# Optimization experiments

Hardware: AMD Instinct MI355X
Metric: run time of the kernel (lower is better)

Reference implementation:

```python
import jax, jax.numpy as jnp
import numpy as np

N, L, C, H, W, HEAD = 16, 256, 512, 32, 32, 16

def setup_inputs() -> dict:
    key = jax.random.key(0)
    ks = jax.random.split(key, 8)
    s = 0.02  # weight init scale
    return {
        "feature": jax.random.normal(ks[0], (N, C, H, W), jnp.float32),
        "token": jax.random.normal(ks[1], (N, L, C), jnp.float32),
        "wq": jax.random.normal(ks[2], (C, C), jnp.float32) * s,
        "bq": jax.random.normal(ks[3], (C,), jnp.float32) * s,
        "wk": jax.random.normal(ks[4], (C, C), jnp.float32) * s,
        "bk": jax.random.normal(ks[5], (C,), jnp.float32) * s,
        "wv": jax.random.normal(ks[6], (C, C), jnp.float32) * s,
        "bv": jax.random.normal(ks[7], (C,), jnp.float32) * s,
    }

def reference(feature, token, wq, bq, wk, bk, wv, bv):
    n, c, hgt, wid = feature.shape
    h = HEAD
    d = c // h
    l = token.shape[1]
    scale = jnp.asarray(np.sqrt(c / h), feature.dtype)
    tok = token.transpose(0, 2, 1)  # (N, C, L)
    # 1x1 conv projections == per-position GEMMs
    v = (jnp.einsum('ncl,dc->ndl', tok, wv) + bv[None, :, None]).reshape(n, h, d, l)
    k = (jnp.einsum('ncl,dc->ndl', tok, wk) + bk[None, :, None]).reshape(n, h, d, l)
    q = (jnp.einsum('nchw,dc->ndhw', feature, wq) + bq[None, :, None, None])
    q = q.reshape(n, h, d, hgt * wid).transpose(0, 1, 3, 2)  # (N, h, HW, d)
    scores = jnp.einsum('nhqd,nhdl->nhql', q, k) / scale  # (N, h, HW, L)
    coef = jax.nn.softmax(scores, axis=-1)
    proj = jnp.einsum('nhdl,nhql->nhdq', v, coef)  # (N, h, d, HW)
    return feature + proj.reshape(n, c, hgt, wid)
```

## Files before the change

kernel.cpp:

```cpp
#include <hip/hip_runtime.h>
#include <hip/hip_bf16.h>

#define N_ 16
#define L_ 256
#define C_ 512
#define HW_ 1024
#define HEADS_ 16
#define DH_ 32

typedef unsigned short u16;
typedef unsigned int u32;
typedef __attribute__((ext_vector_type(8))) short short8_t;
typedef __attribute__((ext_vector_type(4))) float f32x4;

__device__ __forceinline__ u16 f2bs(float f) {
    union { float f; u32 i; } x; x.f = f;
    u32 r = x.i + 0x7fffu + ((x.i >> 16) & 1u);
    return (u16)(r >> 16);
}
__device__ __forceinline__ u32 cvt_pk_bf16(float lo, float hi) {
    u32 r;
    asm("v_cvt_pk_bf16_f32 %0, %1, %2" : "=v"(r) : "v"(lo), "v"(hi));
    return r;
}
#define AS1(p) (const __attribute__((address_space(1))) void*)(p)
#define AS3(p) (__attribute__((address_space(3))) void*)(p)

__global__ __launch_bounds__(256) void prep_kernel(
    const float* __restrict__ token, const float* __restrict__ wq,
    const float* __restrict__ wk, const float* __restrict__ wv,
    const float* __restrict__ feature,
    u16* __restrict__ tokb, u16* __restrict__ wqb,
    u16* __restrict__ wkb, u16* __restrict__ wvb,
    u16* __restrict__ Ftb)
{
    __shared__ float LT[64][67];
    const int t = threadIdx.x;

    if (blockIdx.x < 2816) {
        const int idx = blockIdx.x * 256 + t;
        const float* s; u16* d; int off;
        if (idx < 524288)            { s = token; d = tokb; off = idx; }
        else if (idx < 524288+65536) { s = wq; d = wqb; off = idx - 524288; }
        else if (idx < 524288+131072){ s = wk; d = wkb; off = idx - 524288 - 65536; }
        else                         { s = wv; d = wvb; off = idx - 524288 - 131072; }
        float4 v = ((const float4*)s)[off];
        ushort4 w;
        w.x = f2bs(v.x); w.y = f2bs(v.y); w.z = f2bs(v.z); w.w = f2bs(v.w);
        ((ushort4*)d)[off] = w;
    } else {
        const int tidx = blockIdx.x - 2816;
        const int pb = tidx & 15, cb = (tidx >> 4) & 7, n = tidx >> 7;
        const int c0 = cb * 64, pos0 = pb * 64;

        #pragma unroll
        for (int r = 0; r < 4; ++r) {
            const int c = r * 16 + (t >> 4);
            const int p = (t & 15) * 4;
            float4 v = *(const float4*)&feature[
                ((size_t)n * C_ + c0 + c) * HW_ + pos0 + p];
            LT[c][p] = v.x; LT[c][p+1] = v.y; LT[c][p+2] = v.z; LT[c][p+3] = v.w;
        }
        __syncthreads();
        #pragma unroll
        for (int rep = 0; rep < 2; ++rep) {
            const int pos = (t >> 3) + rep * 32;
            const int c = (t & 7) * 8;
            u16 tmp[8];
            #pragma unroll
            for (int j = 0; j < 8; ++j) tmp[j] = f2bs(LT[c + j][pos]);
            *(short8_t*)&Ftb[(size_t)(n * HW_ + pos0 + pos) * C_ + c0 + c] =
                *(short8_t*)tmp;
        }
    }
}

__global__ __launch_bounds__(256) void gemm_kernel(
    const u16* __restrict__ Ftb, const u16* __restrict__ tokb,
    const u16* __restrict__ wqb, const u16* __restrict__ wkb,
    const u16* __restrict__ wvb,
    const float* __restrict__ bq, const float* __restrict__ bk,
    const float* __restrict__ bv,
    u16* __restrict__ Qout, u16* __restrict__ Kout, u16* __restrict__ Vt)
{
    __shared__ __align__(16) unsigned char smem[32768];

    const int t = threadIdx.x;
    const int lane = t & 63, wid = t >> 6;
    const int i16 = lane & 15, g = lane >> 4;
    const int wm = wid >> 1, wn = wid & 1;
    const int r8 = t >> 3, gr = t & 7;

    if (blockIdx.x < 256) {
        const int xcd = blockIdx.x & 7, j = blockIdx.x >> 3;
        const int m0 = (xcd * 4 + (j & 3)) * 128;
        const int n0 = (j >> 2) * 64;
        u16* Tok = (u16*)smem;
        u16* Bk  = (u16*)(smem + 16384);
        u16* Bv  = (u16*)(smem + 24576);
        u16 (*LTo)[72] = (u16(*)[72])smem;

        f32x4 ak[4][2], av[4][2];
        #pragma unroll
        for (int mt = 0; mt < 4; ++mt)
            #pragma unroll
            for (int nt = 0; nt < 2; ++nt) {
                ak[mt][nt] = (f32x4){0.f, 0.f, 0.f, 0.f};
                av[mt][nt] = (f32x4){0.f, 0.f, 0.f, 0.f};
            }

        for (int c0 = 0; c0 < C_; c0 += 64) {
            __syncthreads();
            #pragma unroll
            for (int p = 0; p < 4; ++p) {
                const int row = p * 32 + r8;
                __builtin_amdgcn_global_load_lds(
                    AS1(tokb + (size_t)(m0 + row) * C_ + c0 + ((gr ^ (row & 7)) << 3)),
                    AS3(smem + (p * 32 + wid * 8) * 128), 16, 0, 0);
            }
            #pragma unroll
            for (int p = 0; p < 2; ++p) {
                const int row = p * 32 + r8;
                const int gs = (gr ^ (row & 7)) << 3;
                __builtin_amdgcn_global_load_lds(
                    AS1(wkb + (size_t)(n0 + row) * C_ + c0 + gs),
                    AS3(smem + 16384 + (p * 32 + wid * 8) * 128), 16, 0, 0);
                __builtin_amdgcn_global_load_lds(
                    AS1(wvb + (size_t)(n0 + row) * C_ + c0 + gs),
                    AS3(smem + 24576 + (p * 32 + wid * 8) * 128), 16, 0, 0);
            }
            __syncthreads();
            #pragma unroll
            for (int ks = 0; ks < 2; ++ks) {
                short8_t a[4], bbk[2], bbv[2];
                #pragma unroll
                for (int mt = 0; mt < 4; ++mt) {
                    const int m = wm * 64 + mt * 16 + i16;
                    a[mt] = *(const short8_t*)&Tok[m * 64 + ((((ks << 2) | g) ^ (m & 7)) << 3)];
                }
                #pragma unroll
                for (int nt = 0; nt < 2; ++nt) {
                    const int d = wn * 32 + nt * 16 + i16;
                    const int sw = d * 64 + ((((ks << 2) | g) ^ (d & 7)) << 3);
                    bbk[nt] = *(const short8_t*)&Bk[sw];
                    bbv[nt] = *(const short8_t*)&Bv[sw];
                }
                #pragma unroll
                for (int mt = 0; mt < 4; ++mt)
                    #pragma unroll
                    for (int nt = 0; nt < 2; ++nt) {
                        ak[mt][nt] = __builtin_amdgcn_mfma_f32_16x16x32_bf16(
                            a[mt], bbk[nt], ak[mt][nt], 0, 0, 0);
                        av[mt][nt] = __builtin_amdgcn_mfma_f32_16x16x32_bf16(
                            a[mt], bbv[nt], av[mt][nt], 0, 0, 0);
                    }
            }
        }
        const int nb = m0 >> 8, l0 = m0 & 255;
        const size_t vtbase = (size_t)nb * C_ * L_;
        #pragma unroll
        for (int nt = 0; nt < 2; ++nt) {
            const int d = n0 + wn * 32 + nt * 16 + i16;
            const float bb = bv[d];
            #pragma unroll
            for (int mt = 0; mt < 4; ++mt) {
                ushort4 w;
                w.x = f2bs(av[mt][nt][0] + bb);
                w.y = f2bs(av[mt][nt][1] + bb);
                w.z = f2bs(av[mt][nt][2] + bb);
                w.w = f2bs(av[mt][nt][3] + bb);
                const int l = l0 + wm * 64 + mt * 16 + g * 4;
                *(ushort4*)&Vt[vtbase + (size_t)d * L_ + l] = w;
            }
        }
        __syncthreads();
        #pragma unroll
        for (int nt = 0; nt < 2; ++nt) {
            const int col = wn * 32 + nt * 16 + i16;
            const float bb = bk[n0 + col];
            #pragma unroll
            for (int mt = 0; mt < 4; ++mt)
                #pragma unroll
                for (int r = 0; r < 4; ++r)
                    LTo[wm * 64 + mt * 16 + g * 4 + r][col] = f2bs(ak[mt][nt][r] + bb);
        }
        __syncthreads();
        #pragma unroll
        for (int rep = 0; rep < 4; ++rep) {
            const int m = (t >> 3) + rep * 32;
            const int cs = (t & 7) * 8;
            *(short8_t*)&Kout[(size_t)(m0 + m) * C_ + n0 + cs] = *(short8_t*)&LTo[m][cs];
        }
    } else {
        const int qid = blockIdx.x - 256;
        const int xcd = qid & 7, j = qid >> 3;
        const int m0 = (xcd * 16 + (j & 15)) * 128;
        const int n0 = (j >> 4) * 64;
        u16* Ft = (u16*)smem;
        u16* Bq = (u16*)(smem + 16384);
        u16 (*LTo)[72] = (u16(*)[72])smem;

        f32x4 aq[4][2];
        #pragma unroll
        for (int mt = 0; mt < 4; ++mt)
            #pragma unroll
            for (int nt = 0; nt < 2; ++nt)
                aq[mt][nt] = (f32x4){0.f, 0.f, 0.f, 0.f};

        for (int c0 = 0; c0 < C_; c0 += 64) {
            __syncthreads();
            #pragma unroll
            for (int p = 0; p < 4; ++p) {
                const int row = p * 32 + r8;
                __builtin_amdgcn_global_load_lds(
                    AS1(Ftb + (size_t)(m0 + row) * C_ + c0 + ((gr ^ (row & 7)) << 3)),
                    AS3(smem + (p * 32 + wid * 8) * 128), 16, 0, 0);
            }
            #pragma unroll
            for (int p = 0; p < 2; ++p) {
                const int row = p * 32 + r8;
                __builtin_amdgcn_global_load_lds(
                    AS1(wqb + (size_t)(n0 + row) * C_ + c0 + ((gr ^ (row & 7)) << 3)),
                    AS3(smem + 16384 + (p * 32 + wid * 8) * 128), 16, 0, 0);
            }
            __syncthreads();
            #pragma unroll
            for (int ks = 0; ks < 2; ++ks) {
                short8_t a[4], b[2];
                #pragma unroll
                for (int mt = 0; mt < 4; ++mt) {
                    const int m = wm * 64 + mt * 16 + i16;
                    a[mt] = *(const short8_t*)&Ft[m * 64 + ((((ks << 2) | g) ^ (m & 7)) << 3)];
                }
                #pragma unroll
                for (int nt = 0; nt < 2; ++nt) {
                    const int d = wn * 32 + nt * 16 + i16;
                    b[nt] = *(const short8_t*)&Bq[d * 64 + ((((ks << 2) | g) ^ (d & 7)) << 3)];
                }
                #pragma unroll
                for (int mt = 0; mt < 4; ++mt)
                    #pragma unroll
                    for (int nt = 0; nt < 2; ++nt)
                        aq[mt][nt] = __builtin_amdgcn_mfma_f32_16x16x32_bf16(
                            a[mt], b[nt], aq[mt][nt], 0, 0, 0);
            }
        }
        __syncthreads();
        #pragma unroll
        for (int nt = 0; nt < 2; ++nt) {
            const int col = wn * 32 + nt * 16 + i16;
            const float bb = bq[n0 + col];
            #pragma unroll
            for (int mt = 0; mt < 4; ++mt)
                #pragma unroll
                for (int r = 0; r < 4; ++r)
                    LTo[wm * 64 + mt * 16 + g * 4 + r][col] = f2bs(aq[mt][nt][r] + bb);
        }
        __syncthreads();
        #pragma unroll
        for (int rep = 0; rep < 4; ++rep) {
            const int m = (t >> 3) + rep * 32;
            const int cs = (t & 7) * 8;
            *(short8_t*)&Qout[(size_t)(m0 + m) * C_ + n0 + cs] = *(short8_t*)&LTo[m][cs];
        }
    }
}

__global__ __launch_bounds__(256) void attn_kernel(
    const u16* __restrict__ Qws, const u16* __restrict__ Kws,
    const u16* __restrict__ Vws, const float* __restrict__ feature,
    float* __restrict__ out)
{
    __shared__ __align__(16) unsigned char smem[32768];

    const int t = threadIdx.x;
    const int wid = t >> 6, lane = t & 63;
    const int i16 = lane & 15, g = lane >> 4;
    const int pt = blockIdx.x, h = blockIdx.y, n = blockIdx.z;
    const int pos0 = pt * 64;
    const size_t qbase = ((size_t)n * HW_ + pos0) * C_ + h * DH_;
    const size_t kbase = ((size_t)n * L_) * C_ + h * DH_;
    const size_t vbase = (size_t)n * C_ * L_ + (size_t)h * DH_ * L_;

    const int q = wid * 16 + i16;

    short8_t bq = *(const short8_t*)&Qws[qbase + (size_t)q * C_ + g * 8];

    #pragma unroll
    for (int p = 0; p < 4; ++p) {
        const int kg = (lane & 3) ^ ((lane >> 3) & 3);
        const int kr = wid * 64 + p * 16 + (lane >> 2);
        const u16* ksrc = Kws + kbase + (size_t)kr * C_ + kg * 8;
        __builtin_amdgcn_global_load_lds(AS1(ksrc),
            AS3(smem + wid * 4096 + p * 1024), 16, 0, 0);
        const int vd = wid * 8 + p * 2 + (lane >> 5);
        const u16* vsrc = Vws + vbase + (size_t)vd * L_ + ((lane & 31) ^ (vd & 7)) * 8;
        __builtin_amdgcn_global_load_lds(AS1(vsrc),
            AS3(smem + 16384 + wid * 4096 + p * 1024), 16, 0, 0);
    }
    __syncthreads();

    const int kgr = g ^ ((i16 >> 1) & 3);
    f32x4 s[16];
    #pragma unroll
    for (int nf = 0; nf < 16; ++nf) {
        short8_t a = *(const short8_t*)(smem + (nf * 16 + i16) * 64 + kgr * 16);
        f32x4 z = {0.f, 0.f, 0.f, 0.f};
        s[nf] = __builtin_amdgcn_mfma_f32_16x16x32_bf16(a, bq, z, 0, 0, 0);
    }

    float mm[16], sm[16];
    #pragma unroll
    for (int nf = 0; nf < 16; ++nf)
        mm[nf] = fmaxf(fmaxf(s[nf][0], s[nf][1]), fmaxf(s[nf][2], s[nf][3]));
    #pragma unroll
    for (int st = 8; st >= 1; st >>= 1)
        #pragma unroll
        for (int i = 0; i < 8; ++i)
            if (i < st) mm[i] = fmaxf(mm[i], mm[i + st]);
    float m = mm[0];
    m = fmaxf(m, __shfl_xor(m, 16));
    m = fmaxf(m, __shfl_xor(m, 32));

    const float K2 = 0.25506288f;
    #pragma unroll
    for (int nf = 0; nf < 16; ++nf) {
        #pragma unroll
        for (int r = 0; r < 4; ++r) s[nf][r] = exp2f((s[nf][r] - m) * K2);
        sm[nf] = (s[nf][0] + s[nf][1]) + (s[nf][2] + s[nf][3]);
    }
    #pragma unroll
    for (int st = 8; st >= 1; st >>= 1)
        #pragma unroll
        for (int i = 0; i < 8; ++i)
            if (i < st) sm[i] += sm[i + st];
    float ssum = sm[0];
    ssum += __shfl_xor(ssum, 16);
    ssum += __shfl_xor(ssum, 32);
    const float pinv = 1.0f / ssum;

    __syncthreads();

    f32x4 o0 = {0.f, 0.f, 0.f, 0.f}, o1 = {0.f, 0.f, 0.f, 0.f};
    const int e7 = i16 & 7;

    #pragma unroll
    for (int hb = 0; hb < 2; ++hb) {
        #pragma unroll
        for (int nfp = 0; nfp < 8; ++nfp) {
            const int nf = hb * 8 + nfp;
            #pragma unroll
            for (int w = 0; w < 2; ++w) {
                u32 pw = cvt_pk_bf16(s[nf][2 * w] * pinv, s[nf][2 * w + 1] * pinv);
                const int gran = (nfp * 2 + (g >> 1)) ^ e7;
                *(u32*)(smem + q * 256 + gran * 16 + ((g & 1) * 2 + w) * 4) = pw;
            }
        }
        __syncthreads();
        #pragma unroll
        for (int ks = 0; ks < 4; ++ks) {
            short8_t pb = *(const short8_t*)(smem + q * 256 + (((ks * 4 + g) ^ e7) * 16));
            const int vg = (((hb * 4 + ks) * 4 + g) ^ e7) * 16;
            short8_t va0 = *(const short8_t*)(smem + 16384 + i16 * 512 + vg);
            short8_t va1 = *(const short8_t*)(smem + 16384 + (16 + i16) * 512 + vg);
            o0 = __builtin_amdgcn_mfma_f32_16x16x32_bf16(va0, pb, o0, 0, 0, 0);
            o1 = __builtin_amdgcn_mfma_f32_16x16x32_bf16(va1, pb, o1, 0, 0, 0);
        }
        if (hb == 0) __syncthreads();
    }

    const size_t obase = ((size_t)n * C_ + h * DH_) * HW_ + pos0 + q;
    #pragma unroll
    for (int r = 0; r < 4; ++r) {
        const size_t oa = obase + (size_t)(g * 4 + r) * HW_;
        out[oa] = feature[oa] + o0[r];
        const size_t ob = obase + (size_t)(16 + g * 4 + r) * HW_;
        out[ob] = feature[ob] + o1[r];
    }
}

extern "C" void kernel_launch(void* const* d_in, const int* in_sizes, int n_in,
                              void* d_out, int out_size, void* d_ws, size_t ws_size,
                              hipStream_t stream)
{
    const float* feature = (const float*)d_in[0];
    const float* token   = (const float*)d_in[1];
    const float* wq      = (const float*)d_in[2];
    const float* bq      = (const float*)d_in[3];
    const float* wk      = (const float*)d_in[4];
    const float* bk      = (const float*)d_in[5];
    const float* wv      = (const float*)d_in[6];
    const float* bv      = (const float*)d_in[7];
    float* out = (float*)d_out;

    u16* Qws = (u16*)d_ws;
    u16* Kws = Qws + (size_t)N_ * HW_ * C_;
    u16* Vws = Kws + (size_t)N_ * L_ * C_;

    char* ob = (char*)d_out;
    u16* Ftb  = (u16*)ob;
    u16* tokb = (u16*)(ob + (16u << 20));
    u16* wkb  = (u16*)(ob + (20u << 20));
    u16* wvb  = (u16*)(ob + (20u << 20) + 524288);
    u16* wqb  = (u16*)(ob + (21u << 20));

    prep_kernel<<<dim3(4864), 256, 0, stream>>>(token, wq, wk, wv, feature,
                                                tokb, wqb, wkb, wvb, Ftb);
    gemm_kernel<<<dim3(1280), 256, 0, stream>>>(Ftb, tokb, wqb, wkb, wvb,
                                                bq, bk, bv, Qws, Kws, Vws);
    attn_kernel<<<dim3(16, 16, 16), 256, 0, stream>>>(Qws, Kws, Vws, feature, out);
}
```

Baseline: 71.04 us.

## Double-buffer LDS staging in projection GEMM and widen Q tiles to 128

The K/V and Q projection loops now use two 32KB LDS buffers. The next 64-wide channel slice is issued with global_load_lds while MFMAs run on the current slice, which removes one barrier per iteration and hides load latency. The Q branch also doubles its output tile width from 64 to 128 columns, with 16 accumulators per wave. This halves the number of Q blocks (1024 to 512, grid 1280 to 768) and improves reuse of the feature tile. In exchange, LDS per block doubles to 64KB and register pressure rises, which lowers occupancy, and the Q epilogue is split into two halves through LDS.

```diff
diff --git a/kernel.cpp b/kernel.cpp
--- a/kernel.cpp
+++ b/kernel.cpp
@@ -83,21 +83,18 @@
     const float* __restrict__ bv,
     u16* __restrict__ Qout, u16* __restrict__ Kout, u16* __restrict__ Vt)
 {
-    __shared__ __align__(16) unsigned char smem[32768];
+    __shared__ __align__(16) unsigned char smem[65536];
 
     const int t = threadIdx.x;
     const int lane = t & 63, wid = t >> 6;
     const int i16 = lane & 15, g = lane >> 4;
-    const int wm = wid >> 1, wn = wid & 1;
     const int r8 = t >> 3, gr = t & 7;
 
     if (blockIdx.x < 256) {
         const int xcd = blockIdx.x & 7, j = blockIdx.x >> 3;
         const int m0 = (xcd * 4 + (j & 3)) * 128;
         const int n0 = (j >> 2) * 64;
-        u16* Tok = (u16*)smem;
-        u16* Bk  = (u16*)(smem + 16384);
-        u16* Bv  = (u16*)(smem + 24576);
+        const int wm = wid >> 1, wn = wid & 1;
         u16 (*LTo)[72] = (u16(*)[72])smem;
 
         f32x4 ak[4][2], av[4][2];
@@ -109,27 +106,33 @@
                 av[mt][nt] = (f32x4){0.f, 0.f, 0.f, 0.f};
             }
 
-        for (int c0 = 0; c0 < C_; c0 += 64) {
-            __syncthreads();
-            #pragma unroll
-            for (int p = 0; p < 4; ++p) {
-                const int row = p * 32 + r8;
-                __builtin_amdgcn_global_load_lds(
-                    AS1(tokb + (size_t)(m0 + row) * C_ + c0 + ((gr ^ (row & 7)) << 3)),
-                    AS3(smem + (p * 32 + wid * 8) * 128), 16, 0, 0);
-            }
-            #pragma unroll
-            for (int p = 0; p < 2; ++p) {
-                const int row = p * 32 + r8;
-                const int gs = (gr ^ (row & 7)) << 3;
-                __builtin_amdgcn_global_load_lds(
-                    AS1(wkb + (size_t)(n0 + row) * C_ + c0 + gs),
-                    AS3(smem + 16384 + (p * 32 + wid * 8) * 128), 16, 0, 0);
-                __builtin_amdgcn_global_load_lds(
-                    AS1(wvb + (size_t)(n0 + row) * C_ + c0 + gs),
-                    AS3(smem + 24576 + (p * 32 + wid * 8) * 128), 16, 0, 0);
-            }
-            __syncthreads();
+        #define KV_STAGE(buf, c0) { \
+            _Pragma("unroll") \
+            for (int p = 0; p < 4; ++p) { \
+                const int row = p * 32 + r8; \
+                __builtin_amdgcn_global_load_lds( \
+                    AS1(tokb + (size_t)(m0 + row) * C_ + (c0) + ((gr ^ (row & 7)) << 3)), \
+                    AS3(smem + (buf) * 32768 + (p * 32 + wid * 8) * 128), 16, 0, 0); } \
+            _Pragma("unroll") \
+            for (int p = 0; p < 2; ++p) { \
+                const int row = p * 32 + r8; \
+                const int gs = (gr ^ (row & 7)) << 3; \
+                __builtin_amdgcn_global_load_lds( \
+                    AS1(wkb + (size_t)(n0 + row) * C_ + (c0) + gs), \
+                    AS3(smem + (buf) * 32768 + 16384 + (p * 32 + wid * 8) * 128), 16, 0, 0); \
+                __builtin_amdgcn_global_load_lds( \
+                    AS1(wvb + (size_t)(n0 + row) * C_ + (c0) + gs), \
+                    AS3(smem + (buf) * 32768 + 24576 + (p * 32 + wid * 8) * 128), 16, 0, 0); } }
+
+        KV_STAGE(0, 0);
+        __syncthreads();
+        #pragma unroll
+        for (int cs = 0; cs < 8; ++cs) {
+            const int cur = cs & 1;
+            if (cs < 7) KV_STAGE(cur ^ 1, (cs + 1) * 64);
+            const u16* Tok = (const u16*)(smem + cur * 32768);
+            const u16* Bk  = (const u16*)(smem + cur * 32768 + 16384);
+            const u16* Bv  = (const u16*)(smem + cur * 32768 + 24576);
             #pragma unroll
             for (int ks = 0; ks < 2; ++ks) {
                 short8_t a[4], bbk[2], bbv[2];
@@ -155,6 +158,7 @@
                             a[mt], bbv[nt], av[mt][nt], 0, 0, 0);
                     }
             }
+            __syncthreads();
         }
         const int nb = m0 >> 8, l0 = m0 & 255;
         const size_t vtbase = (size_t)nb * C_ * L_;
@@ -188,80 +192,89 @@
         #pragma unroll
         for (int rep = 0; rep < 4; ++rep) {
             const int m = (t >> 3) + rep * 32;
-            const int cs = (t & 7) * 8;
-            *(short8_t*)&Kout[(size_t)(m0 + m) * C_ + n0 + cs] = *(short8_t*)&LTo[m][cs];
+            const int cs2 = (t & 7) * 8;
+            *(short8_t*)&Kout[(size_t)(m0 + m) * C_ + n0 + cs2] = *(short8_t*)&LTo[m][cs2];
         }
     } else {
         const int qid = blockIdx.x - 256;
-        const int xcd = qid & 7, j = qid >> 3;
-        const int m0 = (xcd * 16 + (j & 15)) * 128;
-        const int n0 = (j >> 4) * 64;
-        u16* Ft = (u16*)smem;
-        u16* Bq = (u16*)(smem + 16384);
-        u16 (*LTo)[72] = (u16(*)[72])smem;
-
-        f32x4 aq[4][2];
+        const int xcd = qid & 7, loc = qid >> 3;
+        const int m0 = (xcd * 16 + (loc & 15)) * 128;
+        const int n0 = (loc >> 4) * 128;
+        const int wm = wid >> 1, wn = wid & 1;
+        u16 (*LTo)[136] = (u16(*)[136])smem;
+
+        f32x4 aq[4][4];
         #pragma unroll
         for (int mt = 0; mt < 4; ++mt)
             #pragma unroll
-            for (int nt = 0; nt < 2; ++nt)
+            for (int nt = 0; nt < 4; ++nt)
                 aq[mt][nt] = (f32x4){0.f, 0.f, 0.f, 0.f};
 
-        for (int c0 = 0; c0 < C_; c0 += 64) {
-            __syncthreads();
-            #pragma unroll
-            for (int p = 0; p < 4; ++p) {
-                const int row = p * 32 + r8;
-                __builtin_amdgcn_global_load_lds(
-                    AS1(Ftb + (size_t)(m0 + row) * C_ + c0 + ((gr ^ (row & 7)) << 3)),
-                    AS3(smem + (p * 32 + wid * 8) * 128), 16, 0, 0);
-            }
-            #pragma unroll
-            for (int p = 0; p < 2; ++p) {
-                const int row = p * 32 + r8;
-                __builtin_amdgcn_global_load_lds(
-                    AS1(wqb + (size_t)(n0 + row) * C_ + c0 + ((gr ^ (row & 7)) << 3)),
-                    AS3(smem + 16384 + (p * 32 + wid * 8) * 128), 16, 0, 0);
-            }
-            __syncthreads();
+        #define Q_STAGE(buf, c0) { \
+            _Pragma("unroll") \
+            for (int p = 0; p < 4; ++p) { \
+                const int row = p * 32 + r8; \
+                const int gs = (gr ^ (row & 7)) << 3; \
+                __builtin_amdgcn_global_load_lds( \
+                    AS1(Ftb + (size_t)(m0 + row) * C_ + (c0) + gs), \
+                    AS3(smem + (buf) * 32768 + (p * 32 + wid * 8) * 128), 16, 0, 0); \
+                __builtin_amdgcn_global_load_lds( \
+                    AS1(wqb + (size_t)(n0 + row) * C_ + (c0) + gs), \
+                    AS3(smem + (buf) * 32768 + 16384 + (p * 32 + wid * 8) * 128), 16, 0, 0); } }
+
+        Q_STAGE(0, 0);
+        __syncthreads();
+        #pragma unroll
+        for (int cs = 0; cs < 8; ++cs) {
+            const int cur = cs & 1;
+            if (cs < 7) Q_STAGE(cur ^ 1, (cs + 1) * 64);
+            const u16* Ft = (const u16*)(smem + cur * 32768);
+            const u16* Bq = (const u16*)(smem + cur * 32768 + 16384);
             #pragma unroll
             for (int ks = 0; ks < 2; ++ks) {
-                short8_t a[4], b[2];
+                short8_t a[4], b[4];
                 #pragma unroll
                 for (int mt = 0; mt < 4; ++mt) {
                     const int m = wm * 64 + mt * 16 + i16;
                     a[mt] = *(const short8_t*)&Ft[m * 64 + ((((ks << 2) | g) ^ (m & 7)) << 3)];
                 }
                 #pragma unroll
-                for (int nt = 0; nt < 2; ++nt) {
-                    const int d = wn * 32 + nt * 16 + i16;
+                for (int nt = 0; nt < 4; ++nt) {
+                    const int d = wn * 64 + nt * 16 + i16;
                     b[nt] = *(const short8_t*)&Bq[d * 64 + ((((ks << 2) | g) ^ (d & 7)) << 3)];
                 }
                 #pragma unroll
                 for (int mt = 0; mt < 4; ++mt)
                     #pragma unroll
-                    for (int nt = 0; nt < 2; ++nt)
+                    for (int nt = 0; nt < 4; ++nt)
                         aq[mt][nt] = __builtin_amdgcn_mfma_f32_16x16x32_bf16(
                             a[mt], b[nt], aq[mt][nt], 0, 0, 0);
             }
-        }
-        __syncthreads();
-        #pragma unroll
-        for (int nt = 0; nt < 2; ++nt) {
-            const int col = wn * 32 + nt * 16 + i16;
-            const float bb = bq[n0 + col];
-            #pragma unroll
-            for (int mt = 0; mt < 4; ++mt)
-                #pragma unroll
-                for (int r = 0; r < 4; ++r)
-                    LTo[wm * 64 + mt * 16 + g * 4 + r][col] = f2bs(aq[mt][nt][r] + bb);
-        }
-        __syncthreads();
-        #pragma unroll
-        for (int rep = 0; rep < 4; ++rep) {
-            const int m = (t >> 3) + rep * 32;
-            const int cs = (t & 7) * 8;
-            *(short8_t*)&Qout[(size_t)(m0 + m) * C_ + n0 + cs] = *(short8_t*)&LTo[m][cs];
+            __syncthreads();
+        }
+        #pragma unroll
+        for (int half = 0; half < 2; ++half) {
+            __syncthreads();
+            if (wm == half) {
+                #pragma unroll
+                for (int nt = 0; nt < 4; ++nt) {
+                    const int col = wn * 64 + nt * 16 + i16;
+                    const float bb = bq[n0 + col];
+                    #pragma unroll
+                    for (int mt = 0; mt < 4; ++mt)
+                        #pragma unroll
+                        for (int r = 0; r < 4; ++r)
+                            LTo[mt * 16 + g * 4 + r][col] = f2bs(aq[mt][nt][r] + bb);
+                }
+            }
+            __syncthreads();
+            #pragma unroll
+            for (int rep = 0; rep < 4; ++rep) {
+                const int row = rep * 16 + (t >> 4);
+                const int col = (t & 15) * 8;
+                *(short8_t*)&Qout[(size_t)(m0 + half * 64 + row) * C_ + n0 + col] =
+                    *(short8_t*)&LTo[row][col];
+            }
         }
     }
 }
@@ -406,7 +419,7 @@
 
     prep_kernel<<<dim3(4864), 256, 0, stream>>>(token, wq, wk, wv, feature,
                                                 tokb, wqb, wkb, wvb, Ftb);
-    gemm_kernel<<<dim3(1280), 256, 0, stream>>>(Ftb, tokb, wqb, wkb, wvb,
-                                                bq, bk, bv, Qws, Kws, Vws);
+    gemm_kernel<<<dim3(768), 256, 0, stream>>>(Ftb, tokb, wqb, wkb, wvb,
+                                               bq, bk, bv, Qws, Kws, Vws);
     attn_kernel<<<dim3(16, 16, 16), 256, 0, stream>>>(Qws, Kws, Vws, feature, out);
 }
```

Result: no change. 71.43 us (+0.5%).
